# Performance work log

Hardware: AMD Instinct MI355X
Metric: run time of the kernel (lower is better)

The kernel has to match this reference:

```python
import jax, jax.numpy as jnp
import numpy as np
import math

HEADS = 8
DIM_HEAD = 64
DIM = HEADS * DIM_HEAD  # 512; to_v is Identity so dim must equal heads*dim_head
SCALE = DIM_HEAD ** -0.5


def get_slopes(n):
    def pow2(n):
        start = 2 ** (-2 ** (-(math.log2(n) - 3)))
        return [start * start ** i for i in range(n)]
    if math.log2(n).is_integer():
        return pow2(n)
    c = 2 ** math.floor(math.log2(n))
    return pow2(c) + get_slopes(2 * c)[0::2][: n - c]

SLOPES = jnp.asarray(np.array(get_slopes(HEADS), dtype=np.float32))


def setup_inputs() -> dict:
    key = jax.random.key(0)
    k1, k2, k3, k4 = jax.random.split(key, 4)
    b, n = 4, 2048
    x = jax.random.normal(k1, (b, n, DIM), dtype=jnp.float32)
    # positions: e.g. observation timestamps (days); uniform floats scaled to [0, 365)
    positions = jax.random.uniform(k2, (b, n), dtype=jnp.float32) * 365.0
    Wq = jax.random.normal(k3, (DIM, DIM), dtype=jnp.float32) * (DIM ** -0.5)
    Wk = jax.random.normal(k4, (DIM, DIM), dtype=jnp.float32) * (DIM ** -0.5)
    return {"x": x, "positions": positions, "Wq": Wq, "Wk": Wk}


def reference(x, positions, Wq, Wk):
    b, n, _ = x.shape
    # q, k projections (no bias); v = x (Identity)
    q = (x @ Wq.T).reshape(b, n, HEADS, DIM_HEAD).transpose(0, 2, 1, 3)  # b h n d
    k = (x @ Wk.T).reshape(b, n, HEADS, DIM_HEAD).transpose(0, 2, 1, 3)
    v = x.reshape(b, n, HEADS, DIM_HEAD).transpose(0, 2, 1, 3)
    dots = jnp.einsum('bhid,bhjd->bhij', q, k) * SCALE  # b h n n
    # relative_positions[b,i,j] = -|positions[b,j] - positions[b,i]|
    rel = -jnp.abs(positions[:, None, :] - positions[:, :, None])  # b n n
    alibi = SLOPES[None, :, None, None] * rel[:, None, :, :]  # b h n n
    attn = jax.nn.softmax(dots + alibi, axis=-1)
    out = jnp.einsum('bhij,bhjd->bhid', attn, v)  # b h n d
    return out.transpose(0, 2, 1, 3).reshape(b, n, DIM)
```

## Files before the change

kernel.cpp:

```cpp
#include <hip/hip_runtime.h>
#include <hip/hip_bf16.h>

typedef __bf16 bf16x8 __attribute__((ext_vector_type(8)));
typedef float f32x4 __attribute__((ext_vector_type(4)));
typedef float f32x16 __attribute__((ext_vector_type(16)));

__device__ inline unsigned short f2bf(float f) {
    __hip_bfloat16 h = __float2bfloat16(f);
    return __builtin_bit_cast(unsigned short, h);
}
__device__ inline unsigned pk2bf(float a, float b) {
    return (unsigned)f2bf(a) | ((unsigned)f2bf(b) << 16);
}
__device__ inline float exp2_fast(float x) {
    float r;
    asm("v_exp_f32 %0, %1" : "=v"(r) : "v"(x));
    return r;
}

#define QSCALE 0.1803368801111244f

__global__ __launch_bounds__(256) void xpose_v(const float* __restrict__ x,
                                               unsigned short* __restrict__ Vt) {
    const int tid = threadIdx.x;
    const int lane = tid & 63, w = tid >> 6;
    const int b = blockIdx.z, h = blockIdx.y;
    const int n = blockIdx.x * 256 + w * 64 + lane;
    const size_t xrow = ((size_t)b * 2048 + n) * 512 + h * 64;
    const size_t vbase = ((size_t)(b * 8 + h) * 64) * 2048 + n;
#pragma unroll
    for (int d0 = 0; d0 < 64; d0 += 4) {
        float4 v = *reinterpret_cast<const float4*>(&x[xrow + d0]);
        Vt[vbase + (size_t)(d0 + 0) * 2048] = f2bf(v.x);
        Vt[vbase + (size_t)(d0 + 1) * 2048] = f2bf(v.y);
        Vt[vbase + (size_t)(d0 + 2) * 2048] = f2bf(v.z);
        Vt[vbase + (size_t)(d0 + 3) * 2048] = f2bf(v.w);
    }
}

__global__ __launch_bounds__(256) void gemm_qk(const float* __restrict__ x,
                                               const float* __restrict__ Wq,
                                               const float* __restrict__ Wk,
                                               unsigned short* __restrict__ Qb,
                                               unsigned short* __restrict__ Kb) {
    __shared__ __align__(16) unsigned short sA[128 * 40];
    __shared__ __align__(16) unsigned short sB[128 * 40];
    const int tid  = threadIdx.x;
    const int lane = tid & 63;
    const int wave = tid >> 6;
    const int wr = wave >> 1, wc = wave & 1;
    const int bm = blockIdx.x * 128;
    const int by = blockIdx.y;
    const float* __restrict__ Bsrc = (by < 4) ? Wq : Wk;
    unsigned short* __restrict__ C = (by < 4) ? Qb : Kb;
    const int bn = (by & 3) * 128;
    const float scale = (by < 4) ? QSCALE : 1.0f;
    const int tr = tid >> 1, th = (tid & 1) * 16;
    const int rl = lane & 15;
    const int kq = (lane >> 4) * 8;

    f32x4 acc[4][4];
#pragma unroll
    for (int m = 0; m < 4; ++m)
#pragma unroll
        for (int n = 0; n < 4; ++n) acc[m][n] = (f32x4){0.f, 0.f, 0.f, 0.f};

    for (int k0 = 0; k0 < 512; k0 += 32) {
        const float* ap = &x[(size_t)(bm + tr) * 512 + k0 + th];
        const float* bp = &Bsrc[(size_t)(bn + tr) * 512 + k0 + th];
        float4 a0 = *reinterpret_cast<const float4*>(ap);
        float4 a1 = *reinterpret_cast<const float4*>(ap + 4);
        float4 a2 = *reinterpret_cast<const float4*>(ap + 8);
        float4 a3 = *reinterpret_cast<const float4*>(ap + 12);
        float4 b0 = *reinterpret_cast<const float4*>(bp);
        float4 b1 = *reinterpret_cast<const float4*>(bp + 4);
        float4 b2 = *reinterpret_cast<const float4*>(bp + 8);
        float4 b3 = *reinterpret_cast<const float4*>(bp + 12);
        uint4 pa0 = {pk2bf(a0.x, a0.y), pk2bf(a0.z, a0.w), pk2bf(a1.x, a1.y), pk2bf(a1.z, a1.w)};
        uint4 pa1 = {pk2bf(a2.x, a2.y), pk2bf(a2.z, a2.w), pk2bf(a3.x, a3.y), pk2bf(a3.z, a3.w)};
        uint4 pb0 = {pk2bf(b0.x, b0.y), pk2bf(b0.z, b0.w), pk2bf(b1.x, b1.y), pk2bf(b1.z, b1.w)};
        uint4 pb1 = {pk2bf(b2.x, b2.y), pk2bf(b2.z, b2.w), pk2bf(b3.x, b3.y), pk2bf(b3.z, b3.w)};
        __syncthreads();
        *reinterpret_cast<uint4*>(&sA[tr * 40 + th])     = pa0;
        *reinterpret_cast<uint4*>(&sA[tr * 40 + th + 8]) = pa1;
        *reinterpret_cast<uint4*>(&sB[tr * 40 + th])     = pb0;
        *reinterpret_cast<uint4*>(&sB[tr * 40 + th + 8]) = pb1;
        __syncthreads();

        bf16x8 af[4], bfv[4];
#pragma unroll
        for (int m = 0; m < 4; ++m)
            af[m] = __builtin_bit_cast(bf16x8,
                *reinterpret_cast<const uint4*>(&sA[(wr * 64 + m * 16 + rl) * 40 + kq]));
#pragma unroll
        for (int n = 0; n < 4; ++n)
            bfv[n] = __builtin_bit_cast(bf16x8,
                *reinterpret_cast<const uint4*>(&sB[(wc * 64 + n * 16 + rl) * 40 + kq]));
#pragma unroll
        for (int m = 0; m < 4; ++m)
#pragma unroll
            for (int n = 0; n < 4; ++n)
                acc[m][n] = __builtin_amdgcn_mfma_f32_16x16x32_bf16(af[m], bfv[n], acc[m][n], 0, 0, 0);
    }

    const int rq = (lane >> 4) * 4;
#pragma unroll
    for (int m = 0; m < 4; ++m) {
        int r = bm + wr * 64 + m * 16 + rq;
#pragma unroll
        for (int n = 0; n < 4; ++n) {
            int c = bn + wc * 64 + n * 16 + rl;
#pragma unroll
            for (int reg = 0; reg < 4; ++reg)
                C[(size_t)(r + reg) * 512 + c] = f2bf(acc[m][n][reg] * scale);
        }
    }
}

__global__ __launch_bounds__(512, 4) void attn_fwd(const unsigned short* __restrict__ Q,
                                                   const unsigned short* __restrict__ Kb,
                                                   const unsigned short* __restrict__ Vt,
                                                   const float* __restrict__ pos,
                                                   float* __restrict__ Out) {
    __shared__ __align__(16) unsigned char smem[51456];
    unsigned short* sK = (unsigned short*)smem;
    unsigned short* sV = (unsigned short*)(smem + 8192);
    float* sPos = (float*)(smem + 16384);
    float* sM   = (float*)(smem + 16640);

    const int tid  = threadIdx.x;
    const int lane = tid & 63;
    const int w    = tid >> 6;
    const int l31  = lane & 31;
    const int hi   = lane >> 5;
    const int qh   = w & 3;
    const int jp   = w >> 2;
    const int b = blockIdx.z, h = blockIdx.y;
    const int q0 = blockIdx.x * 128 + qh * 32;
    const size_t rowbase = (size_t)b * 2048;
    const int hc = h * 64;
    const int bh = b * 8 + h;
    const float slopeL = ldexpf(1.4426950408889634f, -(h + 1));

    bf16x8 qf0, qf1, qf2, qf3;
    {
        const unsigned short* qp = &Q[(rowbase + q0 + l31) * 512 + hc + hi * 8];
        qf0 = __builtin_bit_cast(bf16x8, *reinterpret_cast<const uint4*>(qp));
        qf1 = __builtin_bit_cast(bf16x8, *reinterpret_cast<const uint4*>(qp + 16));
        qf2 = __builtin_bit_cast(bf16x8, *reinterpret_cast<const uint4*>(qp + 32));
        qf3 = __builtin_bit_cast(bf16x8, *reinterpret_cast<const uint4*>(qp + 48));
    }
    const float ui = slopeL * pos[rowbase + q0 + l31];

    float lloc = 0.f;
    f32x16 o0, o1;
#pragma unroll
    for (int r = 0; r < 16; ++r) { o0[r] = 0.f; o1[r] = 0.f; }

    const int sr  = tid >> 3;
    const int sqe = (tid & 7) * 8;
    const int wbyte = sr * 128 + (((tid & 7) * 16) ^ ((sr & 7) << 4));
    const int kswz = (l31 & 7) << 4;
    const char* sKrow = (const char*)sK + (32 * jp + l31) * 128;
    const char* sVr0  = (const char*)sV + l31 * 128;
    const char* sVr1  = (const char*)sV + (32 + l31) * 128;
    const int vb = 64 * jp;

    uint4 ck, cv;
    float cpj = 0.f;
    {
        ck = *reinterpret_cast<const uint4*>(&Kb[(rowbase + sr) * 512 + hc + sqe]);
        cv = *reinterpret_cast<const uint4*>(&Vt[((size_t)bh * 64 + sr) * 2048 + sqe]);
        if (tid < 64) cpj = pos[rowbase + tid];
    }

    for (int j0 = 0; j0 < 2048; j0 += 64) {
        __syncthreads();
        *reinterpret_cast<uint4*>((char*)sK + wbyte) = ck;
        *reinterpret_cast<uint4*>((char*)sV + wbyte) = cv;
        if (tid < 64) sPos[tid] = slopeL * cpj;
        if (j0 + 64 < 2048) {
            ck = *reinterpret_cast<const uint4*>(&Kb[(rowbase + j0 + 64 + sr) * 512 + hc + sqe]);
            cv = *reinterpret_cast<const uint4*>(&Vt[((size_t)bh * 64 + sr) * 2048 + j0 + 64 + sqe]);
            if (tid < 64) cpj = pos[rowbase + j0 + 64 + tid];
        }
        __syncthreads();

        f32x16 s;
#pragma unroll
        for (int r = 0; r < 16; ++r) s[r] = 0.f;
        __builtin_amdgcn_s_setprio(1);
#pragma unroll
        for (int ks = 0; ks < 4; ++ks) {
            bf16x8 kf = __builtin_bit_cast(bf16x8,
                *reinterpret_cast<const uint4*>(sKrow + ((ks * 32 + hi * 16) ^ kswz)));
            bf16x8 qq = (ks == 0) ? qf0 : (ks == 1) ? qf1 : (ks == 2) ? qf2 : qf3;
            s = __builtin_amdgcn_mfma_f32_32x32x16_bf16(kf, qq, s, 0, 0, 0);
        }
        __builtin_amdgcn_s_setprio(0);

        float ls = 0.f;
#pragma unroll
        for (int t = 0; t < 4; ++t) {
            f32x4 u = *reinterpret_cast<const f32x4*>(&sPos[32 * jp + 8 * t + 4 * hi]);
#pragma unroll
            for (int r = 0; r < 4; ++r) {
                float v = s[4 * t + r] - fabsf(u[r] - ui);
                float p = exp2_fast(v);
                s[4 * t + r] = p;
                ls += p;
            }
        }
        lloc += ls;

        bf16x8 pf0 = __builtin_bit_cast(bf16x8, (uint4){
            pk2bf(s[0], s[1]),  pk2bf(s[2], s[3]),   pk2bf(s[4], s[5]),   pk2bf(s[6], s[7])});
        bf16x8 pf1 = __builtin_bit_cast(bf16x8, (uint4){
            pk2bf(s[8], s[9]),  pk2bf(s[10], s[11]), pk2bf(s[12], s[13]), pk2bf(s[14], s[15])});

        __builtin_amdgcn_s_setprio(1);
#pragma unroll
        for (int ks = 0; ks < 2; ++ks) {
            const int cb = vb + ks * 32 + hi * 8;
            uint2 a0 = *reinterpret_cast<const uint2*>(sVr0 + (cb ^ kswz));
            uint2 a1 = *reinterpret_cast<const uint2*>(sVr0 + ((cb + 16) ^ kswz));
            uint2 b0 = *reinterpret_cast<const uint2*>(sVr1 + (cb ^ kswz));
            uint2 b1 = *reinterpret_cast<const uint2*>(sVr1 + ((cb + 16) ^ kswz));
            bf16x8 v0 = __builtin_bit_cast(bf16x8, (uint4){a0.x, a0.y, a1.x, a1.y});
            bf16x8 v1 = __builtin_bit_cast(bf16x8, (uint4){b0.x, b0.y, b1.x, b1.y});
            bf16x8 pf = ks ? pf1 : pf0;
            o0 = __builtin_amdgcn_mfma_f32_32x32x16_bf16(v0, pf, o0, 0, 0, 0);
            o1 = __builtin_amdgcn_mfma_f32_32x32x16_bf16(v1, pf, o1, 0, 0, 0);
        }
        __builtin_amdgcn_s_setprio(0);
    }

    float lt = lloc + __shfl_xor(lloc, 32, 64);
    __syncthreads();
    if (w >= 4) {
        float* dst = sM + (size_t)(w - 4) * 2048 + lane * 32;
        const int key = (lane & 7) << 2;
#pragma unroll
        for (int i = 0; i < 4; ++i) {
            f32x4 t0 = {o0[4 * i], o0[4 * i + 1], o0[4 * i + 2], o0[4 * i + 3]};
            f32x4 t1 = {o1[4 * i], o1[4 * i + 1], o1[4 * i + 2], o1[4 * i + 3]};
            *reinterpret_cast<f32x4*>(dst + ((4 * i) ^ key))      = t0;
            *reinterpret_cast<f32x4*>(dst + ((16 + 4 * i) ^ key)) = t1;
        }
        sM[8192 + (w - 4) * 64 + lane] = lt;
    }
    __syncthreads();
    float linv = 0.f;
    if (w < 4) {
        const float* src = sM + (size_t)w * 2048 + lane * 32;
        const int key = (lane & 7) << 2;
#pragma unroll
        for (int i = 0; i < 4; ++i) {
            f32x4 t0 = *reinterpret_cast<const f32x4*>(src + ((4 * i) ^ key));
            f32x4 t1 = *reinterpret_cast<const f32x4*>(src + ((16 + 4 * i) ^ key));
#pragma unroll
            for (int r = 0; r < 4; ++r) { o0[4 * i + r] += t0[r]; o1[4 * i + r] += t1[r]; }
        }
        linv = 1.0f / (lt + sM[8192 + w * 64 + lane]);
    }
    __syncthreads();
    if (w < 4) {
        float* sO = sM + w * (32 * 68);
#pragma unroll
        for (int t = 0; t < 4; ++t) {
            f32x4 v0, v1;
#pragma unroll
            for (int r = 0; r < 4; ++r) {
                v0[r] = o0[4 * t + r] * linv;
                v1[r] = o1[4 * t + r] * linv;
            }
            *reinterpret_cast<f32x4*>(&sO[l31 * 68 + 8 * t + 4 * hi])      = v0;
            *reinterpret_cast<f32x4*>(&sO[l31 * 68 + 32 + 8 * t + 4 * hi]) = v1;
        }
#pragma unroll
        for (int rr = 0; rr < 8; ++rr) {
            int qr = rr * 4 + (lane >> 4);
            int ch = lane & 15;
            f32x4 v = *reinterpret_cast<const f32x4*>(&sO[qr * 68 + ch * 4]);
            *reinterpret_cast<f32x4*>(&Out[(rowbase + q0 + qr) * 512 + hc + ch * 4]) = v;
        }
    }
}

extern "C" void kernel_launch(void* const* d_in, const int* in_sizes, int n_in,
                              void* d_out, int out_size, void* d_ws, size_t ws_size,
                              hipStream_t stream) {
    const float* x   = (const float*)d_in[0];
    const float* pos = (const float*)d_in[1];
    const float* Wq  = (const float*)d_in[2];
    const float* Wk  = (const float*)d_in[3];
    float* out = (float*)d_out;

    unsigned short* Qb  = (unsigned short*)d_ws;
    unsigned short* Kbf = Qb  + 4194304;
    unsigned short* Vtb = Kbf + 4194304;

    xpose_v<<<dim3(8, 8, 4), dim3(256), 0, stream>>>(x, Vtb);
    gemm_qk<<<dim3(64, 8), dim3(256), 0, stream>>>(x, Wq, Wk, Qb, Kbf);
    attn_fwd<<<dim3(16, 8, 4), dim3(512), 0, stream>>>(Qb, Kbf, Vtb, pos, out);
}
```

Measured before the change: 89.28 us.

## Double-buffer K/V tiles and halve attention block to 256 threads

Shrinks the attention block from 8 to 4 waves (64 query rows per block, grid doubled) and double-buffers the K/V/position tiles in LDS. This halves the barriers per key tile and overlaps global loads with compute. The epilogue now writes output straight from registers instead of staging through LDS, trading coalescing for one fewer barrier. Each thread now loads more data per stage, which increases register pressure. K/V tiles are reloaded by twice as many blocks.

After: 99.53 us. +11.5%, slower.

```diff
diff --git a/kernel.cpp b/kernel.cpp
--- a/kernel.cpp
+++ b/kernel.cpp
@@ -117,26 +117,28 @@
     }
 }
 
-__global__ __launch_bounds__(512, 4) void attn_fwd(const unsigned short* __restrict__ Q,
+__global__ __launch_bounds__(256, 4) void attn_fwd(const unsigned short* __restrict__ Q,
                                                    const unsigned short* __restrict__ Kb,
                                                    const unsigned short* __restrict__ Vt,
                                                    const float* __restrict__ pos,
                                                    float* __restrict__ Out) {
-    __shared__ __align__(16) unsigned char smem[51456];
-    unsigned short* sK = (unsigned short*)smem;
-    unsigned short* sV = (unsigned short*)(smem + 8192);
-    float* sPos = (float*)(smem + 16384);
-    float* sM   = (float*)(smem + 16640);
+    __shared__ __align__(16) unsigned char smem[33280];
+    char* k0b = (char*)smem;
+    char* v0b = (char*)smem + 8192;
+    char* k1b = (char*)smem + 16384;
+    char* v1b = (char*)smem + 24576;
+    float* p0b = (float*)(smem + 32768);
+    float* p1b = (float*)(smem + 33024);
 
     const int tid  = threadIdx.x;
     const int lane = tid & 63;
     const int w    = tid >> 6;
     const int l31  = lane & 31;
     const int hi   = lane >> 5;
-    const int qh   = w & 3;
-    const int jp   = w >> 2;
+    const int qh   = w & 1;
+    const int jp   = w >> 1;
     const int b = blockIdx.z, h = blockIdx.y;
-    const int q0 = blockIdx.x * 128 + qh * 32;
+    const int q0 = blockIdx.x * 64 + qh * 32;
     const size_t rowbase = (size_t)b * 2048;
     const int hc = h * 64;
     const int bh = b * 8 + h;
@@ -157,35 +159,34 @@
 #pragma unroll
     for (int r = 0; r < 16; ++r) { o0[r] = 0.f; o1[r] = 0.f; }
 
-    const int sr  = tid >> 3;
-    const int sqe = (tid & 7) * 8;
-    const int wbyte = sr * 128 + (((tid & 7) * 16) ^ ((sr & 7) << 4));
+    const int sr  = tid >> 2;
+    const int sce = (tid & 3) * 16;
+    const int swk = (sr & 7) << 4;
+    const int wb0 = sr * 128 + (((tid & 3) * 32) ^ swk);
+    const int wb1 = sr * 128 + ((((tid & 3) * 32) + 16) ^ swk);
     const int kswz = (l31 & 7) << 4;
-    const char* sKrow = (const char*)sK + (32 * jp + l31) * 128;
-    const char* sVr0  = (const char*)sV + l31 * 128;
-    const char* sVr1  = (const char*)sV + (32 + l31) * 128;
-    const int vb = 64 * jp;
-
-    uint4 ck, cv;
+
+    uint4 ck0, ck1, cv0, cv1;
     float cpj = 0.f;
-    {
-        ck = *reinterpret_cast<const uint4*>(&Kb[(rowbase + sr) * 512 + hc + sqe]);
-        cv = *reinterpret_cast<const uint4*>(&Vt[((size_t)bh * 64 + sr) * 2048 + sqe]);
-        if (tid < 64) cpj = pos[rowbase + tid];
-    }
-
-    for (int j0 = 0; j0 < 2048; j0 += 64) {
-        __syncthreads();
-        *reinterpret_cast<uint4*>((char*)sK + wbyte) = ck;
-        *reinterpret_cast<uint4*>((char*)sV + wbyte) = cv;
-        if (tid < 64) sPos[tid] = slopeL * cpj;
-        if (j0 + 64 < 2048) {
-            ck = *reinterpret_cast<const uint4*>(&Kb[(rowbase + j0 + 64 + sr) * 512 + hc + sqe]);
-            cv = *reinterpret_cast<const uint4*>(&Vt[((size_t)bh * 64 + sr) * 2048 + j0 + 64 + sqe]);
-            if (tid < 64) cpj = pos[rowbase + j0 + 64 + tid];
-        }
-        __syncthreads();
-
+
+    auto stage = [&](int j0v) {
+        const unsigned short* kp = &Kb[(rowbase + j0v + sr) * 512 + hc + sce];
+        const unsigned short* vp = &Vt[((size_t)bh * 64 + sr) * 2048 + j0v + sce];
+        ck0 = *reinterpret_cast<const uint4*>(kp);
+        ck1 = *reinterpret_cast<const uint4*>(kp + 8);
+        cv0 = *reinterpret_cast<const uint4*>(vp);
+        cv1 = *reinterpret_cast<const uint4*>(vp + 8);
+        if (tid < 64) cpj = pos[rowbase + j0v + tid];
+    };
+    auto writeb = [&](char* KB, char* VB, float* PB) {
+        *reinterpret_cast<uint4*>(KB + wb0) = ck0;
+        *reinterpret_cast<uint4*>(KB + wb1) = ck1;
+        *reinterpret_cast<uint4*>(VB + wb0) = cv0;
+        *reinterpret_cast<uint4*>(VB + wb1) = cv1;
+        if (tid < 64) PB[tid] = slopeL * cpj;
+    };
+    auto compute = [&](const char* KB, const char* VB, const float* PB) {
+        const char* kr = KB + (32 * jp + l31) * 128;
         f32x16 s;
 #pragma unroll
         for (int r = 0; r < 16; ++r) s[r] = 0.f;
@@ -193,7 +194,7 @@
 #pragma unroll
         for (int ks = 0; ks < 4; ++ks) {
             bf16x8 kf = __builtin_bit_cast(bf16x8,
-                *reinterpret_cast<const uint4*>(sKrow + ((ks * 32 + hi * 16) ^ kswz)));
+                *reinterpret_cast<const uint4*>(kr + ((ks * 32 + hi * 16) ^ kswz)));
             bf16x8 qq = (ks == 0) ? qf0 : (ks == 1) ? qf1 : (ks == 2) ? qf2 : qf3;
             s = __builtin_amdgcn_mfma_f32_32x32x16_bf16(kf, qq, s, 0, 0, 0);
         }
@@ -202,11 +203,10 @@
         float ls = 0.f;
 #pragma unroll
         for (int t = 0; t < 4; ++t) {
-            f32x4 u = *reinterpret_cast<const f32x4*>(&sPos[32 * jp + 8 * t + 4 * hi]);
+            f32x4 u = *reinterpret_cast<const f32x4*>(&PB[32 * jp + 8 * t + 4 * hi]);
 #pragma unroll
             for (int r = 0; r < 4; ++r) {
-                float v = s[4 * t + r] - fabsf(u[r] - ui);
-                float p = exp2_fast(v);
+                float p = exp2_fast(s[4 * t + r] - fabsf(u[r] - ui));
                 s[4 * t + r] = p;
                 ls += p;
             }
@@ -218,14 +218,16 @@
         bf16x8 pf1 = __builtin_bit_cast(bf16x8, (uint4){
             pk2bf(s[8], s[9]),  pk2bf(s[10], s[11]), pk2bf(s[12], s[13]), pk2bf(s[14], s[15])});
 
+        const char* vr0 = VB + l31 * 128;
+        const char* vr1 = VB + (32 + l31) * 128;
         __builtin_amdgcn_s_setprio(1);
 #pragma unroll
         for (int ks = 0; ks < 2; ++ks) {
-            const int cb = vb + ks * 32 + hi * 8;
-            uint2 a0 = *reinterpret_cast<const uint2*>(sVr0 + (cb ^ kswz));
-            uint2 a1 = *reinterpret_cast<const uint2*>(sVr0 + ((cb + 16) ^ kswz));
-            uint2 b0 = *reinterpret_cast<const uint2*>(sVr1 + (cb ^ kswz));
-            uint2 b1 = *reinterpret_cast<const uint2*>(sVr1 + ((cb + 16) ^ kswz));
+            const int cb = 64 * jp + ks * 32 + hi * 8;
+            uint2 a0 = *reinterpret_cast<const uint2*>(vr0 + (cb ^ kswz));
+            uint2 a1 = *reinterpret_cast<const uint2*>(vr0 + ((cb + 16) ^ kswz));
+            uint2 b0 = *reinterpret_cast<const uint2*>(vr1 + (cb ^ kswz));
+            uint2 b1 = *reinterpret_cast<const uint2*>(vr1 + ((cb + 16) ^ kswz));
             bf16x8 v0 = __builtin_bit_cast(bf16x8, (uint4){a0.x, a0.y, a1.x, a1.y});
             bf16x8 v1 = __builtin_bit_cast(bf16x8, (uint4){b0.x, b0.y, b1.x, b1.y});
             bf16x8 pf = ks ? pf1 : pf0;
@@ -233,13 +235,32 @@
             o1 = __builtin_amdgcn_mfma_f32_32x32x16_bf16(v1, pf, o1, 0, 0, 0);
         }
         __builtin_amdgcn_s_setprio(0);
+    };
+
+    stage(0);
+    writeb(k0b, v0b, p0b);
+    stage(64);
+    __syncthreads();
+
+    for (int t = 0; t < 32; t += 2) {
+        writeb(k1b, v1b, p1b);
+        if (t + 2 < 32) stage((t + 2) * 64);
+        compute(k0b, v0b, p0b);
+        __syncthreads();
+        if (t + 2 < 32) {
+            writeb(k0b, v0b, p0b);
+            if (t + 3 < 32) stage((t + 3) * 64);
+        }
+        compute(k1b, v1b, p1b);
+        __syncthreads();
     }
 
     float lt = lloc + __shfl_xor(lloc, 32, 64);
-    __syncthreads();
-    if (w >= 4) {
-        float* dst = sM + (size_t)(w - 4) * 2048 + lane * 32;
-        const int key = (lane & 7) << 2;
+    float* sM  = (float*)smem;
+    float* sMl = sM + 4096;
+    const int key = (lane & 7) << 2;
+    if (jp == 1) {
+        float* dst = sM + qh * 2048 + lane * 32;
 #pragma unroll
         for (int i = 0; i < 4; ++i) {
             f32x4 t0 = {o0[4 * i], o0[4 * i + 1], o0[4 * i + 2], o0[4 * i + 3]};
@@ -247,13 +268,11 @@
             *reinterpret_cast<f32x4*>(dst + ((4 * i) ^ key))      = t0;
             *reinterpret_cast<f32x4*>(dst + ((16 + 4 * i) ^ key)) = t1;
         }
-        sM[8192 + (w - 4) * 64 + lane] = lt;
+        sMl[qh * 64 + lane] = lt;
     }
     __syncthreads();
-    float linv = 0.f;
-    if (w < 4) {
-        const float* src = sM + (size_t)w * 2048 + lane * 32;
-        const int key = (lane & 7) << 2;
+    if (jp == 0) {
+        const float* src = sM + qh * 2048 + lane * 32;
 #pragma unroll
         for (int i = 0; i < 4; ++i) {
             f32x4 t0 = *reinterpret_cast<const f32x4*>(src + ((4 * i) ^ key));
@@ -261,28 +280,18 @@
 #pragma unroll
             for (int r = 0; r < 4; ++r) { o0[4 * i + r] += t0[r]; o1[4 * i + r] += t1[r]; }
         }
-        linv = 1.0f / (lt + sM[8192 + w * 64 + lane]);
-    }
-    __syncthreads();
-    if (w < 4) {
-        float* sO = sM + w * (32 * 68);
+        const float linv = 1.0f / (lt + sMl[qh * 64 + lane]);
+        float* orow = &Out[(rowbase + q0 + l31) * 512 + hc];
 #pragma unroll
         for (int t = 0; t < 4; ++t) {
-            f32x4 v0, v1;
+            f32x4 a, c;
 #pragma unroll
             for (int r = 0; r < 4; ++r) {
-                v0[r] = o0[4 * t + r] * linv;
-                v1[r] = o1[4 * t + r] * linv;
+                a[r] = o0[4 * t + r] * linv;
+                c[r] = o1[4 * t + r] * linv;
             }
-            *reinterpret_cast<f32x4*>(&sO[l31 * 68 + 8 * t + 4 * hi])      = v0;
-            *reinterpret_cast<f32x4*>(&sO[l31 * 68 + 32 + 8 * t + 4 * hi]) = v1;
-        }
-#pragma unroll
-        for (int rr = 0; rr < 8; ++rr) {
-            int qr = rr * 4 + (lane >> 4);
-            int ch = lane & 15;
-            f32x4 v = *reinterpret_cast<const f32x4*>(&sO[qr * 68 + ch * 4]);
-            *reinterpret_cast<f32x4*>(&Out[(rowbase + q0 + qr) * 512 + hc + ch * 4]) = v;
+            *reinterpret_cast<f32x4*>(orow + 8 * t + 4 * hi)      = a;
+            *reinterpret_cast<f32x4*>(orow + 32 + 8 * t + 4 * hi) = c;
         }
     }
 }
@@ -302,5 +311,5 @@
 
     xpose_v<<<dim3(8, 8, 4), dim3(256), 0, stream>>>(x, Vtb);
     gemm_qk<<<dim3(64, 8), dim3(256), 0, stream>>>(x, Wq, Wk, Qb, Kbf);
-    attn_fwd<<<dim3(16, 8, 4), dim3(512), 0, stream>>>(Qb, Kbf, Vtb, pos, out);
-}
+    attn_fwd<<<dim3(32, 8, 4), dim3(256), 0, stream>>>(Qb, Kbf, Vtb, pos, out);
+}
```
